# Optimization experiments

Measured on AMD Instinct MI355X. Metric: run time of the kernel, lower is better.

The kernel has to match this reference:

```python
import jax, jax.numpy as jnp
import numpy as np


def _make_kernels():
    # 4 fixed 3x3x3 stencils: identity + Sobel x/y/z (separable smooth x smooth x derivative)
    d = np.array([-1.0, 0.0, 1.0], dtype=np.float32)
    s = np.array([1.0, 2.0, 1.0], dtype=np.float32)
    sx = np.einsum('i,j,k->ijk', s, s, d) / 16.0
    sy = np.einsum('i,j,k->ijk', s, d, s) / 16.0
    sz = np.einsum('i,j,k->ijk', d, s, s) / 16.0
    ident = np.zeros((3, 3, 3), dtype=np.float32)
    ident[1, 1, 1] = 1.0
    return np.stack([ident, sx, sy, sz], axis=0)  # (4,3,3,3)


def setup_inputs() -> dict:
    key = jax.random.key(0)
    x = jax.random.normal(key, (4, 16, 64, 64, 64), dtype=jnp.float32)
    kernels = jnp.asarray(_make_kernels())  # fixed buffer, (4,3,3,3)
    return {"x": x, "kernels": kernels}


def reference(x, kernels):
    B, C, D, H, W = x.shape
    # replicate padding by 1 on each spatial side
    xp = jnp.pad(x, ((0, 0), (0, 0), (1, 1), (1, 1), (1, 1)), mode='edge')
    # depthwise: every channel gets all 4 filters -> fold channels into batch,
    # run one conv with 4 output channels, then restore torch's [k*C + c] ordering
    xr = xp.reshape(B * C, 1, D + 2, H + 2, W + 2)
    k = kernels[:, None]  # (4,1,3,3,3), OIDHW
    out = jax.lax.conv_general_dilated(
        xr, k, window_strides=(1, 1, 1), padding='VALID',
        dimension_numbers=('NCDHW', 'OIDHW', 'NCDHW'))  # (B*C,4,D,H,W)
    out = out.reshape(B, C, 4, D, H, W).transpose(0, 2, 1, 3, 4, 5)
    return out.reshape(B, 4 * C, D, H, W)
```

## Files before the change

kernel.cpp:

```cpp
#include <hip/hip_runtime.h>


#define B_ 4
#define C_ 16
#define D_ 64
#define H_ 64
#define W_ 64

typedef float float4v __attribute__((ext_vector_type(4)));

__global__ __launch_bounds__(256) void perceive3d_kernel(
    const float* __restrict__ x, float* __restrict__ out)
{
    const int lane = threadIdx.x;
    const int quad = lane & 15;
    const int hsub = lane >> 4;
    const int h    = blockIdx.x * 16 + threadIdx.y * 4 + hsub;
    const int d    = blockIdx.y;
    const int bc   = blockIdx.z;
    const int b    = bc >> 4;
    const int c    = bc & 15;

    const float* xb = x + (size_t)bc * (D_ * H_ * W_);

    const int dm = (d == 0) ? 0 : d - 1;
    const int dp = (d == D_ - 1) ? D_ - 1 : d + 1;
    const int hm = (h == 0) ? 0 : h - 1;
    const int hp = (h == H_ - 1) ? H_ - 1 : h + 1;

    const int dzo[3] = { dm * (H_ * W_), d * (H_ * W_), dp * (H_ * W_) };
    const int hyo[3] = { hm * W_,        h * W_,        hp * W_ };
    const float si[3] = { 1.0f, 2.0f, 1.0f };

    float4v sx = {0,0,0,0}, sy = {0,0,0,0}, sz = {0,0,0,0};
    float4v center = {0,0,0,0};

#pragma unroll
    for (int i = 0; i < 3; ++i) {
#pragma unroll
        for (int j = 0; j < 3; ++j) {
            const float* row = xb + dzo[i] + hyo[j];
            float4v q = *(const float4v*)(row + 4 * quad);

            float left  = __shfl_up(q.w, 1);
            float right = __shfl_down(q.x, 1);
            if (quad == 0)      left  = q.x;
            if (quad == 15)     right = q.w;

            float4v am = { left, q.x, q.y, q.z };
            float4v ap = { q.y, q.z, q.w, right };

            float4v sw = am + 2.0f * q + ap;
            float4v dw = ap - am;

            const float cij = si[i] * si[j];
            sx += cij * dw;
            if (j == 0)      sy -= si[i] * sw;
            else if (j == 2) sy += si[i] * sw;
            if (i == 0)      sz -= si[j] * sw;
            else if (i == 2) sz += si[j] * sw;
            if (i == 1 && j == 1) center = q;
        }
    }

    sx *= (1.0f / 16.0f);
    sy *= (1.0f / 16.0f);
    sz *= (1.0f / 16.0f);

    const size_t dhw     = (size_t)D_ * H_ * W_;
    const size_t cdhw    = (size_t)C_ * dhw;
    const size_t spatial = ((size_t)d * H_ + h) * W_ + 4 * quad;

    float* o = out + ((size_t)(b * 4) * C_ + c) * dhw + spatial;
    __builtin_nontemporal_store(center, (float4v*)(o + 0 * cdhw));
    __builtin_nontemporal_store(sx,     (float4v*)(o + 1 * cdhw));
    __builtin_nontemporal_store(sy,     (float4v*)(o + 2 * cdhw));
    __builtin_nontemporal_store(sz,     (float4v*)(o + 3 * cdhw));
}

extern "C" void kernel_launch(void* const* d_in, const int* in_sizes, int n_in,
                              void* d_out, int out_size, void* d_ws, size_t ws_size,
                              hipStream_t stream) {
    (void)in_sizes; (void)n_in; (void)d_ws; (void)ws_size; (void)out_size;
    const float* x = (const float*)d_in[0];
    float* out = (float*)d_out;

    dim3 block(64, 4, 1);
    dim3 grid(H_ / 16, D_, B_ * C_);
    perceive3d_kernel<<<grid, block, 0, stream>>>(x, out);
}
```

Baseline: 314.1 us.

## March each thread through depth chunks, reusing separable plane partials

Each thread now walks DCHUNK=8 consecutive depth slices, keeping a rolling window of three per-plane separable partial sums (smooth/derivative along W and H) in registers. This replaces the 9 row loads and the full 27-tap accumulation per output with 3 new row loads and one plane computation per step. The aim is to cut redundant global/L2 reads and ALU work. The grid shrinks by a factor of 8 in depth, which lowers parallelism and latency hiding on a kernel that is mostly bound by write bandwidth.

```diff
diff --git a/kernel.cpp b/kernel.cpp
--- a/kernel.cpp
+++ b/kernel.cpp
@@ -6,8 +6,34 @@
 #define D_ 64
 #define H_ 64
 #define W_ 64
+#define DCHUNK 8
 
 typedef float float4v __attribute__((ext_vector_type(4)));
+
+__device__ __forceinline__ void row_uv(float4v q, int quad, float4v& u, float4v& v)
+{
+    float left  = __shfl_up(q.w, 1);
+    float right = __shfl_down(q.x, 1);
+    if (quad == 0)  left  = q.x;
+    if (quad == 15) right = q.w;
+    float4v am = { left, q.x, q.y, q.z };
+    float4v ap = { q.y, q.z, q.w, right };
+    u = am + 2.0f * q + ap;
+    v = ap - am;
+}
+
+__device__ __forceinline__ void make_plane(float4v qm, float4v qc, float4v qp,
+                                           int quad,
+                                           float4v& A, float4v& Bv, float4v& Cc)
+{
+    float4v um, vm, uc, vc, up, vp;
+    row_uv(qm, quad, um, vm);
+    row_uv(qc, quad, uc, vc);
+    row_uv(qp, quad, up, vp);
+    A  = um + 2.0f * uc + up;
+    Bv = vm + 2.0f * vc + vp;
+    Cc = up - um;
+}
 
 __global__ __launch_bounds__(256) void perceive3d_kernel(
     const float* __restrict__ x, float* __restrict__ out)
@@ -16,66 +42,77 @@
     const int quad = lane & 15;
     const int hsub = lane >> 4;
     const int h    = blockIdx.x * 16 + threadIdx.y * 4 + hsub;
-    const int d    = blockIdx.y;
+    const int d0   = blockIdx.y * DCHUNK;
     const int bc   = blockIdx.z;
     const int b    = bc >> 4;
     const int c    = bc & 15;
 
-    const float* xb = x + (size_t)bc * (D_ * H_ * W_);
+    const float* xb = x + (size_t)bc * (D_ * H_ * W_) + 4 * quad;
 
-    const int dm = (d == 0) ? 0 : d - 1;
-    const int dp = (d == D_ - 1) ? D_ - 1 : d + 1;
     const int hm = (h == 0) ? 0 : h - 1;
     const int hp = (h == H_ - 1) ? H_ - 1 : h + 1;
+    const int rm = hm * W_;
+    const int rc = h  * W_;
+    const int rp = hp * W_;
 
-    const int dzo[3] = { dm * (H_ * W_), d * (H_ * W_), dp * (H_ * W_) };
-    const int hyo[3] = { hm * W_,        h * W_,        hp * W_ };
-    const float si[3] = { 1.0f, 2.0f, 1.0f };
+    float4v A0, Bv0, Cc0, A1, Bv1, Cc1, q1;
+    float4v m0, m1, m2;
 
-    float4v sx = {0,0,0,0}, sy = {0,0,0,0}, sz = {0,0,0,0};
-    float4v center = {0,0,0,0};
+    {
+        const float* p0 = xb + ((d0 == 0) ? 0 : d0 - 1) * (H_ * W_);
+        float4v a  = *(const float4v*)(p0 + rm);
+        float4v bq = *(const float4v*)(p0 + rc);
+        float4v cq = *(const float4v*)(p0 + rp);
+        make_plane(a, bq, cq, quad, A0, Bv0, Cc0);
+
+        const float* p1 = xb + d0 * (H_ * W_);
+        a  = *(const float4v*)(p1 + rm);
+        bq = *(const float4v*)(p1 + rc);
+        cq = *(const float4v*)(p1 + rp);
+        make_plane(a, bq, cq, quad, A1, Bv1, Cc1);
+        q1 = bq;
+
+        const int dn = (d0 + 1 > D_ - 1) ? D_ - 1 : d0 + 1;
+        const float* p2 = xb + dn * (H_ * W_);
+        m0 = *(const float4v*)(p2 + rm);
+        m1 = *(const float4v*)(p2 + rc);
+        m2 = *(const float4v*)(p2 + rp);
+    }
+
+    const size_t dhw  = (size_t)D_ * H_ * W_;
+    const size_t cdhw = (size_t)C_ * dhw;
+    float* o = out + ((size_t)(b * 4) * C_ + c) * dhw
+                   + ((size_t)d0 * H_ + h) * W_ + 4 * quad;
 
 #pragma unroll
-    for (int i = 0; i < 3; ++i) {
-#pragma unroll
-        for (int j = 0; j < 3; ++j) {
-            const float* row = xb + dzo[i] + hyo[j];
-            float4v q = *(const float4v*)(row + 4 * quad);
+    for (int t = 0; t < DCHUNK; ++t) {
+        const int d = d0 + t;
 
-            float left  = __shfl_up(q.w, 1);
-            float right = __shfl_down(q.x, 1);
-            if (quad == 0)      left  = q.x;
-            if (quad == 15)     right = q.w;
+        float4v nqm = m0, nqc = m1, nqp = m2;
 
-            float4v am = { left, q.x, q.y, q.z };
-            float4v ap = { q.y, q.z, q.w, right };
+        const int dn = (d + 2 > D_ - 1) ? D_ - 1 : d + 2;
+        const float* pn = xb + dn * (H_ * W_);
+        m0 = *(const float4v*)(pn + rm);
+        m1 = *(const float4v*)(pn + rc);
+        m2 = *(const float4v*)(pn + rp);
 
-            float4v sw = am + 2.0f * q + ap;
-            float4v dw = ap - am;
+        float4v A2, Bv2, Cc2;
+        make_plane(nqm, nqc, nqp, quad, A2, Bv2, Cc2);
 
-            const float cij = si[i] * si[j];
-            sx += cij * dw;
-            if (j == 0)      sy -= si[i] * sw;
-            else if (j == 2) sy += si[i] * sw;
-            if (i == 0)      sz -= si[j] * sw;
-            else if (i == 2) sz += si[j] * sw;
-            if (i == 1 && j == 1) center = q;
-        }
+        float4v sx = (Bv0 + 2.0f * Bv1 + Bv2) * (1.0f / 16.0f);
+        float4v sy = (Cc0 + 2.0f * Cc1 + Cc2) * (1.0f / 16.0f);
+        float4v sz = (A2 - A0)               * (1.0f / 16.0f);
+
+        __builtin_nontemporal_store(q1, (float4v*)(o + 0 * cdhw));
+        __builtin_nontemporal_store(sx, (float4v*)(o + 1 * cdhw));
+        __builtin_nontemporal_store(sy, (float4v*)(o + 2 * cdhw));
+        __builtin_nontemporal_store(sz, (float4v*)(o + 3 * cdhw));
+        o += H_ * W_;
+
+        A0 = A1; Bv0 = Bv1; Cc0 = Cc1;
+        A1 = A2; Bv1 = Bv2; Cc1 = Cc2;
+        q1 = nqc;
     }
-
-    sx *= (1.0f / 16.0f);
-    sy *= (1.0f / 16.0f);
-    sz *= (1.0f / 16.0f);
-
-    const size_t dhw     = (size_t)D_ * H_ * W_;
-    const size_t cdhw    = (size_t)C_ * dhw;
-    const size_t spatial = ((size_t)d * H_ + h) * W_ + 4 * quad;
-
-    float* o = out + ((size_t)(b * 4) * C_ + c) * dhw + spatial;
-    __builtin_nontemporal_store(center, (float4v*)(o + 0 * cdhw));
-    __builtin_nontemporal_store(sx,     (float4v*)(o + 1 * cdhw));
-    __builtin_nontemporal_store(sy,     (float4v*)(o + 2 * cdhw));
-    __builtin_nontemporal_store(sz,     (float4v*)(o + 3 * cdhw));
 }
 
 extern "C" void kernel_launch(void* const* d_in, const int* in_sizes, int n_in,
@@ -86,6 +123,6 @@
     float* out = (float*)d_out;
 
     dim3 block(64, 4, 1);
-    dim3 grid(H_ / 16, D_, B_ * C_);
+    dim3 grid(H_ / 16, D_ / DCHUNK, B_ * C_);
     perceive3d_kernel<<<grid, block, 0, stream>>>(x, out);
 }
```

Result: no change. 317.9 us (+1.2%).
